# Kernel tuning notes

Hardware: AMD Instinct MI355X
Metric: run time of the kernel (lower is better)

Reference implementation:

```python
import jax, jax.numpy as jnp
import numpy as np

H_IMG, W_IMG = 64, 64          # token grid (n = H*W = 4096)
D_MODEL = 512
N_HEADS = 8
D1 = 1024                      # expand_ratio * d_model, multiple of n_heads
HEAD_DIM = D1 // N_HEADS       # 128
RANK = 32
NK = 16                        # inducing points for SKI interpolation


def interp_weights(n, nk):
    # inverse-time warp: position i -> 1/(i+1) in (0,1], linearly interpolated
    # onto nk uniform inducing points in [0,1] (2 nonzeros per row).
    pos = 1.0 / (jnp.arange(n, dtype=jnp.float32) + 1.0)
    t = pos * (nk - 1)
    idx = jnp.clip(jnp.floor(t).astype(jnp.int32), 0, nk - 2)
    frac = t - idx.astype(jnp.float32)
    r = jnp.arange(n)
    Wm = jnp.zeros((n, nk), jnp.float32)
    Wm = Wm.at[r, idx].set(1.0 - frac).at[r, idx + 1].set(frac)
    return Wm  # (n, nk)


def apply_toep(v, U, V):
    # v: (b, m, n, h, d); low-rank SKI Toeplitz mixing along axis n.
    # T ~= (Wm @ U) (Wm @ V)^T per head  -> O(n*r*d) instead of O(n^2*d).
    n = v.shape[2]
    nk = U.shape[1]
    Wm = interp_weights(n, nk)                      # (n, nk)
    A = jnp.einsum('nk,hkr->hnr', Wm, U)            # (h, n, r)
    B = jnp.einsum('nk,hkr->hnr', Wm, V)            # (h, n, r)
    tmp = jnp.einsum('hnr,bmnhd->bmhrd', B, v)      # contract over n
    return jnp.einsum('hnr,bmhrd->bmnhd', A, tmp)


def setup_inputs() -> dict:
    key = jax.random.key(0)
    ks = jax.random.split(key, 12)
    s = 0.02
    x = jax.random.normal(ks[0], (16, H_IMG * W_IMG, D_MODEL), jnp.float32)
    Wu = s * jax.random.normal(ks[1], (D1, D_MODEL), jnp.float32)
    bu = s * jax.random.normal(ks[2], (D1,), jnp.float32)
    Wv = s * jax.random.normal(ks[3], (D1, D_MODEL), jnp.float32)
    bv = s * jax.random.normal(ks[4], (D1,), jnp.float32)
    Wo = s * jax.random.normal(ks[5], (D_MODEL, D1), jnp.float32)
    bo = s * jax.random.normal(ks[6], (D_MODEL,), jnp.float32)
    U1 = s * jax.random.normal(ks[7], (N_HEADS, NK, RANK), jnp.float32)
    V1 = s * jax.random.normal(ks[8], (N_HEADS, NK, RANK), jnp.float32)
    U2 = s * jax.random.normal(ks[9], (N_HEADS, NK, RANK), jnp.float32)
    V2 = s * jax.random.normal(ks[10], (N_HEADS, NK, RANK), jnp.float32)
    return {'x': x, 'Wu': Wu, 'bu': bu, 'Wv': Wv, 'bv': bv, 'Wo': Wo,
            'bo': bo, 'U1': U1, 'V1': V1, 'U2': U2, 'V2': V2}


def reference(x, Wu, bu, Wv, bv, Wo, bo, U1, V1, U2, V2):
    b, n, _ = x.shape
    H = int(np.sqrt(n)); W = n // H
    u = jax.nn.silu(x @ Wu.T + bu)                  # (b, n, d1)
    v = jax.nn.silu(x @ Wv.T + bv)                  # (b, n, d1)
    v4 = v.reshape(b, H, W, N_HEADS, HEAD_DIM)      # (b, H, W, h, d)

    # o1: toep1 along W, then toep2 along H
    t = apply_toep(v4, U1, V1)                      # mix along W
    t = t.transpose(0, 2, 1, 3, 4)                  # (b, W, H, h, d)
    t = apply_toep(t, U2, V2)                       # mix along H
    o1 = t.transpose(0, 2, 1, 3, 4)

    # o2: toep2 along H, then toep1 along W
    s_ = v4.transpose(0, 2, 1, 3, 4)                # (b, W, H, h, d)
    s_ = apply_toep(s_, U2, V2)                     # mix along H
    s_ = s_.transpose(0, 2, 1, 3, 4)                # (b, H, W, h, d)
    o2 = apply_toep(s_, U1, V1)                     # mix along W

    out = (o1 + o2).reshape(b, n, D1)
    out = u * out                                   # gated token mixing
    return out @ Wo.T + bo                          # (b, n, d_model)
```

## Files before the change

### kernel.cpp

```cpp
#include <hip/hip_runtime.h>
#include <hip/hip_bf16.h>

typedef unsigned short u16;
typedef unsigned int   u32;
typedef float  f32x4  __attribute__((ext_vector_type(4)));
typedef __bf16 bf16x8 __attribute__((ext_vector_type(8)));
typedef u16    u16x8  __attribute__((ext_vector_type(8)));
typedef u16    u16x4  __attribute__((ext_vector_type(4)));

__device__ __forceinline__ u16 f2bf(float f) {
  u32 x = __builtin_bit_cast(u32, f);
  x += 0x7fffu + ((x >> 16) & 1u);
  return (u16)(x >> 16);
}
__device__ __forceinline__ float bf2f(u16 u) {
  return __builtin_bit_cast(float, (u32)u << 16);
}
__device__ __forceinline__ void gload_lds16(const u16* g, u16* l) {
  __builtin_amdgcn_global_load_lds(
      (const __attribute__((address_space(1))) void*)g,
      (__attribute__((address_space(3))) void*)l, 16, 0, 0);
}

__global__ void k_conv_x(const float* __restrict__ x, u16* __restrict__ xb) {
  int g = blockIdx.x * 256 + threadIdx.x;
  const float4* src = (const float4*)(x + (size_t)g * 8);
  float4 f0 = src[0], f1 = src[1];
  u16x8 o;
  o[0]=f2bf(f0.x); o[1]=f2bf(f0.y); o[2]=f2bf(f0.z); o[3]=f2bf(f0.w);
  o[4]=f2bf(f1.x); o[5]=f2bf(f1.y); o[6]=f2bf(f1.z); o[7]=f2bf(f1.w);
  *(u16x8*)(xb + (size_t)g * 8) = o;
}

__global__ void k_conv_w(const float* __restrict__ Wu, const float* __restrict__ Wv,
                         const float* __restrict__ Wo, const float* __restrict__ bu,
                         const float* __restrict__ bv, u16* __restrict__ wuvb,
                         u16* __restrict__ wob, float* __restrict__ biasuv) {
  int g = blockIdx.x * 256 + threadIdx.x;
  int e = g * 4;
  const float* src; u16* dst;
  if (e < 524288)        { src = Wu + e;             dst = wuvb + e; }
  else if (e < 1048576)  { src = Wv + (e - 524288);  dst = wuvb + e; }
  else                   { src = Wo + (e - 1048576); dst = wob + (e - 1048576); }
  float4 f = *(const float4*)src;
  u16x4 o; o[0]=f2bf(f.x); o[1]=f2bf(f.y); o[2]=f2bf(f.z); o[3]=f2bf(f.w);
  *(u16x4*)dst = o;
  if (g < 2048) biasuv[g] = (g < 1024) ? bu[g] : bv[g - 1024];
}

__global__ void k_toep(const float* __restrict__ U1, const float* __restrict__ V1,
                       const float* __restrict__ U2, const float* __restrict__ V2,
                       u16* __restrict__ T1b, u16* __restrict__ T2b) {
  __shared__ float Us[512], Vs[512];
  int bid = blockIdx.x, t = threadIdx.x;
  int which = bid >> 6, rest = bid & 63, h = rest >> 3, seg = rest & 7;
  const float* U = which ? U2 : U1;
  const float* V = which ? V2 : V1;
  u16* T = which ? T2b : T1b;
  float scale = which ? 2.0f : 1.0f;
  for (int i = t; i < 512; i += 256) { Us[i] = U[h*512 + i]; Vs[i] = V[h*512 + i]; }
  __syncthreads();
  for (int q = 0; q < 2; ++q) {
    int e = seg * 512 + q * 256 + t;
    int i = e >> 6, j = e & 63;
    float pi = 1.0f / (float)(i + 1); float tvi = pi * 15.0f;
    int ii = min((int)floorf(tvi), 14); float fi = tvi - (float)ii;
    float pj = 1.0f / (float)(j + 1); float tvj = pj * 15.0f;
    int jj = min((int)floorf(tvj), 14); float fj = tvj - (float)jj;
    float s = 0.0f;
    #pragma unroll
    for (int r = 0; r < 32; ++r) {
      float a = (1.0f - fi) * Us[ii*32 + r] + fi * Us[(ii+1)*32 + r];
      float b = (1.0f - fj) * Vs[jj*32 + r] + fj * Vs[(jj+1)*32 + r];
      s += a * b;
    }
    T[h*4096 + i*64 + j] = f2bf(s * scale);
  }
}

template<int EPI>
__global__ __launch_bounds__(512, 2) void k_gemm256(
    const u16* __restrict__ A, const u16* __restrict__ B,
    const float* __restrict__ bias, void* __restrict__ C,
    int K, int nbn, int ldc) {
  extern __shared__ uint4 smem4[];
  u16* lds = (u16*)smem4;
  const int t = threadIdx.x;
  const int l = t & 63, w = t >> 6;
  const int wmi = w >> 2, wni = w & 3;
  const int nwg = gridDim.x;
  const int lb = (blockIdx.x & 7) * (nwg >> 3) + (blockIdx.x >> 3);
  const int bm = lb / nbn, bn = lb % nbn;
  const u16* Ab = A + (size_t)bm * 256 * K;
  const u16* Bb = B + (size_t)bn * 256 * K;
  const int NT = K >> 6;
  const int NOPS = NT * 4;

  f32x4 acc[8][4];
  #pragma unroll
  for (int i = 0; i < 8; ++i)
    #pragma unroll
    for (int j = 0; j < 4; ++j) acc[i][j] = (f32x4){0.f, 0.f, 0.f, 0.f};

#define STAGE(gop) do {                                                      \
    int _g = (gop);                                                          \
    int _tile = _g >> 2, _half = _g & 3;                                     \
    int _kt = _tile << 6;                                                    \
    const u16* _src = (_half < 2) ? Ab : Bb;                                 \
    int _rowbase = (_half & 1) << 7;                                         \
    u16* _dst = lds + (_tile & 1) * 32768 + ((_half >= 2) ? 16384 : 0)       \
                + _rowbase * 64;                                             \
    _Pragma("unroll")                                                        \
    for (int _j = 0; _j < 2; ++_j) {                                         \
      int _idx = _j * 512 + t;                                               \
      int _rr = _idx >> 3, _s8 = _idx & 7;                                   \
      int _R = _rowbase + _rr;                                               \
      int _col = (_s8 ^ (_R & 7)) << 3;                                      \
      gload_lds16(_src + (size_t)_R * K + _kt + _col, _dst + _idx * 8);      \
    }                                                                        \
  } while (0)

  #pragma unroll
  for (int g = 0; g < 7; ++g) STAGE(g);
  asm volatile("s_waitcnt vmcnt(6)");
  __builtin_amdgcn_s_barrier();

  for (int tile = 0; tile < NT; ++tile) {
    const int buf = tile & 1;
    const u16* As = lds + buf * 32768;
    const u16* Bs = As + 16384;
    #pragma unroll
    for (int p = 0; p < 4; ++p) {
      const int mq = (p >> 1) * 4, nq = (p & 1) * 2;
      bf16x8 af[8], bfv[4];
      #pragma unroll
      for (int ks = 0; ks < 2; ++ks) {
        #pragma unroll
        for (int i = 0; i < 4; ++i) {
          int R = (wmi << 7) + (mq + i) * 16 + (l & 15);
          int q8 = ks * 4 + (l >> 4);
          af[ks*4+i] = *(const bf16x8*)&As[R * 64 + ((q8 ^ (R & 7)) << 3)];
        }
        #pragma unroll
        for (int i = 0; i < 2; ++i) {
          int R = (wni << 6) + (nq + i) * 16 + (l & 15);
          int q8 = ks * 4 + (l >> 4);
          bfv[ks*2+i] = *(const bf16x8*)&Bs[R * 64 + ((q8 ^ (R & 7)) << 3)];
        }
      }
      {
        int g = 7 + tile * 4 + p;
        if (g < NOPS) STAGE(g);
      }
      if (p == 3) {
        if (tile < NT - 2)        asm volatile("s_waitcnt vmcnt(6)");
        else if (tile == NT - 2)  asm volatile("s_waitcnt vmcnt(0)");
      }
      __builtin_amdgcn_s_barrier();
      asm volatile("s_waitcnt lgkmcnt(0)");
      __builtin_amdgcn_s_setprio(1);
      #pragma unroll
      for (int ks = 0; ks < 2; ++ks)
        #pragma unroll
        for (int i = 0; i < 4; ++i)
          #pragma unroll
          for (int j = 0; j < 2; ++j)
            acc[mq+i][nq+j] = __builtin_amdgcn_mfma_f32_16x16x32_bf16(
                af[ks*4+i], bfv[ks*2+j], acc[mq+i][nq+j], 0, 0, 0);
      __builtin_amdgcn_s_setprio(0);
      __builtin_amdgcn_s_barrier();
    }
  }
#undef STAGE

  float bcol[4];
  #pragma unroll
  for (int nf = 0; nf < 4; ++nf)
    bcol[nf] = bias[bn * 256 + (wni << 6) + nf * 16 + (l & 15)];
  #pragma unroll
  for (int mf = 0; mf < 8; ++mf) {
    int gm0 = bm * 256 + (wmi << 7) + mf * 16 + (l >> 4) * 4;
    #pragma unroll
    for (int nf = 0; nf < 4; ++nf) {
      int gn = bn * 256 + (wni << 6) + nf * 16 + (l & 15);
      #pragma unroll
      for (int r = 0; r < 4; ++r) {
        float z = acc[mf][nf][r] + bcol[nf];
        size_t off = (size_t)(gm0 + r) * ldc + gn;
        if (EPI == 0) {
          z = z / (1.0f + __expf(-z));
          ((u16*)C)[off] = f2bf(z);
        } else {
          ((float*)C)[off] = z;
        }
      }
    }
  }
}

template<int PASS>
__global__ __launch_bounds__(256) void k_mix(const u16* __restrict__ uv,
                                             u16* __restrict__ y,
                                             const u16* __restrict__ Tmat) {
  __shared__ alignas(16) u16 Ts[64 * 72];
  __shared__ alignas(16) u32 VT[128 * 36];
  int bid = blockIdx.x, t = threadIdx.x;
  int h = bid & 7, outer = (bid >> 3) & 63, b = bid >> 9;
  int l = t & 63, w = t >> 6;

  {
    const u16* Tg = Tmat + h * 4096;
    int rr = t >> 2, cc = (t & 3) * 16;
    const uint4* src = (const uint4*)(Tg + rr * 64 + cc);
    uint4 v0 = src[0], v1 = src[1];
    *(uint4*)&Ts[rr * 72 + cc] = v0;
    *(uint4*)&Ts[rr * 72 + cc + 8] = v1;
  }

  size_t inbase; size_t instride;
  if (PASS == 0) { inbase = ((size_t)(b*64 + outer) * 64) * 2048 + 1024 + h*128; instride = 2048; }
  else           { inbase = ((size_t)b * 4096 + outer) * 1024 + h*128;            instride = 65536; }
  const u16* inp = (PASS == 0) ? uv : (const u16*)y;

  #pragma unroll
  for (int a2 = 0; a2 < 2; ++a2) {
    int jp = (t >> 4) + a2 * 16;
    int dc = t & 15;
    const u16* r0 = inp + inbase + (size_t)(2*jp) * instride + dc * 8;
    const u16* r1 = r0 + instride;
    uint4 av = *(const uint4*)r0;
    uint4 bv = *(const uint4*)r1;
    u32 a4[4] = {av.x, av.y, av.z, av.w};
    u32 b4[4] = {bv.x, bv.y, bv.z, bv.w};
    #pragma unroll
    for (int ww = 0; ww < 4; ++ww) {
      u32 lo = (a4[ww] & 0xffffu) | (b4[ww] << 16);
      u32 hi = (a4[ww] >> 16) | (b4[ww] & 0xffff0000u);
      int d0 = dc * 8 + 2 * ww, d1 = d0 + 1;
      VT[d0 * 36 + (jp ^ ((((u32)d0 >> 3) & 7) << 2))] = lo;
      VT[d1 * 36 + (jp ^ ((((u32)d1 >> 3) & 7) << 2))] = hi;
    }
  }
  __syncthreads();

  f32x4 acc[8];
  #pragma unroll
  for (int nf = 0; nf < 8; ++nf) acc[nf] = (f32x4){0.f, 0.f, 0.f, 0.f};
  #pragma unroll
  for (int ks = 0; ks < 2; ++ks) {
    bf16x8 af = *(const bf16x8*)&Ts[(w*16 + (l & 15)) * 72 + ks*32 + (l >> 4)*8];
    #pragma unroll
    for (int nf = 0; nf < 8; ++nf) {
      int d  = nf * 16 + (l & 15);
      int kd = ks * 16 + (l >> 4) * 4;
      u32 dw = (u32)d * 36 + ((u32)kd ^ ((((u32)d >> 3) & 7) << 2));
      bf16x8 bfv = *(const bf16x8*)&VT[dw];
      acc[nf] = __builtin_amdgcn_mfma_f32_16x16x32_bf16(af, bfv, acc[nf], 0, 0, 0);
    }
  }

  size_t obase, ostride, ubase = 0;
  if (PASS == 0) { obase = ((size_t)(b*64 + outer) * 64) * 1024 + h*128; ostride = 1024; }
  else {
    obase = ((size_t)b * 4096 + outer) * 1024 + h*128; ostride = 65536;
    ubase = ((size_t)b * 4096 + outer) * 2048 + h*128;
  }
  #pragma unroll
  for (int nf = 0; nf < 8; ++nf) {
    int d = nf * 16 + (l & 15);
    #pragma unroll
    for (int r = 0; r < 4; ++r) {
      int m = w * 16 + (l >> 4) * 4 + r;
      float val = acc[nf][r];
      if (PASS == 1) val *= bf2f(uv[ubase + (size_t)m * 131072 + d]);
      y[obase + (size_t)m * ostride + d] = f2bf(val);
    }
  }
}

extern "C" void kernel_launch(void* const* d_in, const int* in_sizes, int n_in,
                              void* d_out, int out_size, void* d_ws, size_t ws_size,
                              hipStream_t stream) {
  const float* x  = (const float*)d_in[0];
  const float* Wu = (const float*)d_in[1];
  const float* bu = (const float*)d_in[2];
  const float* Wv = (const float*)d_in[3];
  const float* bv = (const float*)d_in[4];
  const float* Wo = (const float*)d_in[5];
  const float* bo = (const float*)d_in[6];
  const float* U1 = (const float*)d_in[7];
  const float* V1 = (const float*)d_in[8];
  const float* U2 = (const float*)d_in[9];
  const float* V2 = (const float*)d_in[10];
  float* out = (float*)d_out;

  char* p = (char*)d_ws;
  u16*  xb     = (u16*)(p + 0);
  u16*  wuvb   = (u16*)(p + 67108864);
  u16*  wob    = (u16*)(p + 69206016);
  u16*  T1b    = (u16*)(p + 70254592);
  u16*  T2b    = (u16*)(p + 70320128);
  float* biasuv= (float*)(p + 70385664);
  u16*  uv     = (u16*)(p + 70393856);
  u16*  y      = (u16*)(p + 338829312);
  if (ws_size < 473047040ULL) return;

  (void)hipFuncSetAttribute((const void*)&k_gemm256<0>,
      hipFuncAttributeMaxDynamicSharedMemorySize, 131072);
  (void)hipFuncSetAttribute((const void*)&k_gemm256<1>,
      hipFuncAttributeMaxDynamicSharedMemorySize, 131072);

  k_conv_x<<<16384, 256, 0, stream>>>(x, xb);
  k_conv_w<<<1536, 256, 0, stream>>>(Wu, Wv, Wo, bu, bv, wuvb, wob, biasuv);
  k_toep<<<128, 256, 0, stream>>>(U1, V1, U2, V2, T1b, T2b);
  k_gemm256<0><<<2048, 512, 131072, stream>>>(xb, wuvb, biasuv, (void*)uv, 512, 8, 2048);
  k_mix<0><<<8192, 256, 0, stream>>>(uv, y, T1b);
  k_mix<1><<<8192, 256, 0, stream>>>(uv, y, T2b);
  k_gemm256<1><<<512, 512, 131072, stream>>>(y, wob, bo, (void*)out, 1024, 2, 512);
}
```

Baseline: 546.9 us.

## Reorder GEMM tile ownership and staging schedule to free LDS buffers earlier

Each wave's M rows are split across the two 128-row halves of the A tile instead of one contiguous 128-row block. Each wave loads its B fragments once per K-tile and reuses them across four A phases. The global-to-LDS staging order and vmcnt waits are rescheduled so later-tile loads are issued as soon as the corresponding A-half or B region is no longer needed. The goal is fewer redundant B LDS reads and better overlap of prefetch with MFMA. In exchange, the vmcnt accounting is more intricate and there are more barriers per tile.

```diff
diff --git a/kernel.cpp b/kernel.cpp
--- a/kernel.cpp
+++ b/kernel.cpp
@@ -94,7 +94,6 @@
   const u16* Ab = A + (size_t)bm * 256 * K;
   const u16* Bb = B + (size_t)bn * 256 * K;
   const int NT = K >> 6;
-  const int NOPS = NT * 4;
 
   f32x4 acc[8][4];
   #pragma unroll
@@ -120,72 +119,98 @@
     }                                                                        \
   } while (0)
 
-  #pragma unroll
-  for (int g = 0; g < 7; ++g) STAGE(g);
+#define READ_A(hh, fp) do {                                                  \
+    _Pragma("unroll")                                                        \
+    for (int ks = 0; ks < 2; ++ks)                                           \
+      _Pragma("unroll")                                                      \
+      for (int i = 0; i < 2; ++i) {                                          \
+        int R = ((hh) << 7) + (wmi << 6) + ((fp) * 2 + i) * 16 + (l & 15);   \
+        int q8 = ks * 4 + (l >> 4);                                          \
+        af[ks*2+i] = *(const bf16x8*)&As[R * 64 + ((q8 ^ (R & 7)) << 3)];    \
+      }                                                                      \
+  } while (0)
+
+#define MFMA_PHASE(hh, fp) do {                                              \
+    __builtin_amdgcn_s_setprio(1);                                           \
+    _Pragma("unroll")                                                        \
+    for (int ks = 0; ks < 2; ++ks)                                           \
+      _Pragma("unroll")                                                      \
+      for (int i = 0; i < 2; ++i)                                            \
+        _Pragma("unroll")                                                    \
+        for (int nf = 0; nf < 4; ++nf)                                       \
+          acc[(hh)*4+(fp)*2+i][nf] = __builtin_amdgcn_mfma_f32_16x16x32_bf16(\
+              af[ks*2+i], bfv[ks*4+nf], acc[(hh)*4+(fp)*2+i][nf], 0, 0, 0);  \
+    __builtin_amdgcn_s_setprio(0);                                           \
+  } while (0)
+
+  STAGE(0); STAGE(1); STAGE(2); STAGE(3);
+  STAGE(6); STAGE(7); STAGE(4);
   asm volatile("s_waitcnt vmcnt(6)");
   __builtin_amdgcn_s_barrier();
 
   for (int tile = 0; tile < NT; ++tile) {
-    const int buf = tile & 1;
-    const u16* As = lds + buf * 32768;
+    const u16* As = lds + (tile & 1) * 32768;
     const u16* Bs = As + 16384;
-    #pragma unroll
-    for (int p = 0; p < 4; ++p) {
-      const int mq = (p >> 1) * 4, nq = (p & 1) * 2;
-      bf16x8 af[8], bfv[4];
+    bf16x8 bfv[8];
+    bf16x8 af[4];
+
+    #pragma unroll
+    for (int ks = 0; ks < 2; ++ks)
       #pragma unroll
-      for (int ks = 0; ks < 2; ++ks) {
-        #pragma unroll
-        for (int i = 0; i < 4; ++i) {
-          int R = (wmi << 7) + (mq + i) * 16 + (l & 15);
-          int q8 = ks * 4 + (l >> 4);
-          af[ks*4+i] = *(const bf16x8*)&As[R * 64 + ((q8 ^ (R & 7)) << 3)];
-        }
-        #pragma unroll
-        for (int i = 0; i < 2; ++i) {
-          int R = (wni << 6) + (nq + i) * 16 + (l & 15);
-          int q8 = ks * 4 + (l >> 4);
-          bfv[ks*2+i] = *(const bf16x8*)&Bs[R * 64 + ((q8 ^ (R & 7)) << 3)];
-        }
+      for (int nf = 0; nf < 4; ++nf) {
+        int R = (wni << 6) + nf * 16 + (l & 15);
+        int q8 = ks * 4 + (l >> 4);
+        bfv[ks*4+nf] = *(const bf16x8*)&Bs[R * 64 + ((q8 ^ (R & 7)) << 3)];
       }
-      {
-        int g = 7 + tile * 4 + p;
-        if (g < NOPS) STAGE(g);
-      }
-      if (p == 3) {
-        if (tile < NT - 2)        asm volatile("s_waitcnt vmcnt(6)");
-        else if (tile == NT - 2)  asm volatile("s_waitcnt vmcnt(0)");
-      }
-      __builtin_amdgcn_s_barrier();
-      asm volatile("s_waitcnt lgkmcnt(0)");
-      __builtin_amdgcn_s_setprio(1);
-      #pragma unroll
-      for (int ks = 0; ks < 2; ++ks)
-        #pragma unroll
-        for (int i = 0; i < 4; ++i)
-          #pragma unroll
-          for (int j = 0; j < 2; ++j)
-            acc[mq+i][nq+j] = __builtin_amdgcn_mfma_f32_16x16x32_bf16(
-                af[ks*4+i], bfv[ks*2+j], acc[mq+i][nq+j], 0, 0, 0);
-      __builtin_amdgcn_s_setprio(0);
-      __builtin_amdgcn_s_barrier();
-    }
+    READ_A(0, 0);
+    if (tile + 1 < NT) STAGE(4 * (tile + 1) + 1);
+    __builtin_amdgcn_s_barrier();
+    asm volatile("s_waitcnt lgkmcnt(0)");
+    MFMA_PHASE(0, 0);
+    __builtin_amdgcn_s_barrier();
+
+    READ_A(0, 1);
+    if (tile + 2 < NT) { STAGE(4*(tile+2)+2); STAGE(4*(tile+2)+3); }
+    __builtin_amdgcn_s_barrier();
+    asm volatile("s_waitcnt lgkmcnt(0)");
+    MFMA_PHASE(0, 1);
+    if (tile < NT - 2)       asm volatile("s_waitcnt vmcnt(12)");
+    else if (tile == NT - 2) asm volatile("s_waitcnt vmcnt(8)");
+    else                     asm volatile("s_waitcnt vmcnt(0)");
+    __builtin_amdgcn_s_barrier();
+
+    READ_A(1, 0);
+    if (tile + 2 < NT) STAGE(4 * (tile + 2) + 0);
+    __builtin_amdgcn_s_barrier();
+    asm volatile("s_waitcnt lgkmcnt(0)");
+    MFMA_PHASE(1, 0);
+    __builtin_amdgcn_s_barrier();
+
+    READ_A(1, 1);
+    __builtin_amdgcn_s_barrier();
+    asm volatile("s_waitcnt lgkmcnt(0)");
+    MFMA_PHASE(1, 1);
+    if (tile < NT - 2)       asm volatile("s_waitcnt vmcnt(8)");
+    else if (tile == NT - 2) asm volatile("s_waitcnt vmcnt(2)");
+    __builtin_amdgcn_s_barrier();
   }
 #undef STAGE
+#undef READ_A
+#undef MFMA_PHASE
 
   float bcol[4];
   #pragma unroll
   for (int nf = 0; nf < 4; ++nf)
     bcol[nf] = bias[bn * 256 + (wni << 6) + nf * 16 + (l & 15)];
   #pragma unroll
-  for (int mf = 0; mf < 8; ++mf) {
-    int gm0 = bm * 256 + (wmi << 7) + mf * 16 + (l >> 4) * 4;
+  for (int hf = 0; hf < 8; ++hf) {
+    int gm0 = bm * 256 + (hf >> 2) * 128 + wmi * 64 + (hf & 3) * 16 + (l >> 4) * 4;
     #pragma unroll
     for (int nf = 0; nf < 4; ++nf) {
       int gn = bn * 256 + (wni << 6) + nf * 16 + (l & 15);
       #pragma unroll
       for (int r = 0; r < 4; ++r) {
-        float z = acc[mf][nf][r] + bcol[nf];
+        float z = acc[hf][nf][r] + bcol[nf];
         size_t off = (size_t)(gm0 + r) * ldc + gn;
         if (EPI == 0) {
           z = z / (1.0f + __expf(-z));
```

After: 516.8 us. 1.06x faster.
